# Performance work log

Measured on AMD Instinct MI355X. Metric: run time of the kernel, lower is better.

The kernel has to match this reference:

```python
import jax, jax.numpy as jnp
import numpy as np

N = 100000      # nodes
E = 1600000     # edges (avg degree 16)
F_IN = 64       # in_channels
H = 64          # hidden_channels
L = 3           # num_layers
FINAL = H * L   # jk='cat'


def setup_inputs() -> dict:
    key = jax.random.key(0)
    ks = jax.random.split(key, 16)

    def w(k, i, o):
        return (jax.random.normal(k, (i, o), jnp.float32) / np.sqrt(i)).astype(jnp.float32)

    x = jax.random.normal(ks[0], (N, F_IN), jnp.float32)
    edge_index = jax.random.randint(ks[1], (2, E), 0, N, dtype=jnp.int32)

    inp = {
        'x': x,
        'edge_index': edge_index,
        # layer 1 (in -> H): lin_l (neighbors, with bias), lin_r (root, no bias)
        'W1l': w(ks[2], F_IN, H), 'b1': jnp.zeros((H,), jnp.float32), 'W1r': w(ks[3], F_IN, H),
        # layer 2 (H -> H)
        'W2l': w(ks[4], H, H), 'b2': jnp.zeros((H,), jnp.float32), 'W2r': w(ks[5], H, H),
        # layer 3 (H -> H)
        'W3l': w(ks[6], H, H), 'b3': jnp.zeros((H,), jnp.float32), 'W3r': w(ks[7], H, H),
        # final linear on JK-concat
        'Wlin': w(ks[8], FINAL, 1), 'blin': jnp.zeros((1,), jnp.float32),
    }
    return inp


def _sage_conv(x, src, dst, inv_deg, Wl, bl, Wr):
    # gather neighbor features along edges, segment-mean by destination node
    msg = x[src]                                             # [E, F]
    agg = jax.ops.segment_sum(msg, dst, num_segments=N)      # [N, F]
    agg = agg * inv_deg[:, None]                             # mean aggregation
    return agg @ Wl + bl + x @ Wr                            # lin_l(agg) + lin_r(x)


def reference(x, edge_index, W1l, b1, W1r, W2l, b2, W2r, W3l, b3, W3r, Wlin, blin):
    src, dst = edge_index[0], edge_index[1]
    deg = jax.ops.segment_sum(jnp.ones((E,), jnp.float32), dst, num_segments=N)
    inv_deg = 1.0 / jnp.maximum(deg, 1.0)

    xs = []
    h = x
    for (Wl, bl, Wr) in ((W1l, b1, W1r), (W2l, b2, W2r), (W3l, b3, W3r)):
        h = jax.nn.relu(_sage_conv(h, src, dst, inv_deg, Wl, bl, Wr))
        # dropout is identity in eval mode
        xs.append(h)

    hcat = jnp.concatenate(xs, axis=-1)   # JK 'cat' -> [N, H*L]
    out = hcat @ Wlin + blin              # [N, 1]
    return jax.nn.sigmoid(out).reshape(-1)
```

## Files before the change

### kernel.cpp

```cpp
#include <hip/hip_runtime.h>
#include <math.h>

#define N_NODES 100000
#define N_EDGES 1600000
#define HD 64
#define TILE 128
#define NBUCK 128
#define BNODES 1024
#define EPB 4096

typedef unsigned short ushort_t;
typedef __attribute__((ext_vector_type(8))) unsigned short ushort8_t;
typedef __attribute__((ext_vector_type(8))) short short8_t;
typedef __attribute__((ext_vector_type(4))) float float4_t;

__device__ __forceinline__ float bf2f(ushort_t h){
  union{unsigned u; float f;} v; v.u = ((unsigned)h)<<16; return v.f;
}
__device__ __forceinline__ ushort_t f2bf(float f){
  union{float f; unsigned u;} v; v.f=f;
  unsigned b = v.u + 0x7FFF + ((v.u>>16)&1);
  return (ushort_t)(b>>16);
}

__global__ void k_f32_to_bf16(const float* __restrict__ in, ushort_t* __restrict__ out, int n){
  int i = blockIdx.x*blockDim.x + threadIdx.x;
  int idx = i*4;
  if(idx+3<n){
    float4 v = *(const float4*)&in[idx];
    ushort2 a; a.x=f2bf(v.x); a.y=f2bf(v.y);
    ushort2 b; b.x=f2bf(v.z); b.y=f2bf(v.w);
    *(ushort2*)&out[idx] = a;
    *(ushort2*)&out[idx+2] = b;
  } else {
    for(int k=idx;k<n;k++) out[k]=f2bf(in[k]);
  }
}


__global__ __launch_bounds__(512) void k_hist(const int* __restrict__ dst, int* __restrict__ bcnt, int n){
  __shared__ int lh[NBUCK];
  int t=threadIdx.x;
  if(t<NBUCK) lh[t]=0;
  __syncthreads();
  int base = blockIdx.x*EPB;
  #pragma unroll
  for(int j=0;j<8;j++){
    int e = base + t + j*512;
    if(e<n) atomicAdd(&lh[dst[e]>>10], 1);
  }
  __syncthreads();
  if(t<NBUCK && lh[t]) atomicAdd(&bcnt[t], lh[t]);
}

__global__ void k_scan128(const int* __restrict__ bcnt, int* __restrict__ gcur, int* __restrict__ gbase){
  __shared__ int s[NBUCK];
  int t=threadIdx.x;
  int v=bcnt[t]; s[t]=v;
  __syncthreads();
  for(int off=1; off<NBUCK; off<<=1){
    int a=(t>=off)? s[t-off]:0;
    __syncthreads();
    s[t]+=a;
    __syncthreads();
  }
  int excl = s[t]-v;
  gcur[t]=excl;
  gbase[t]=excl;
  if(t==NBUCK-1) gbase[NBUCK]=s[t];
}

__global__ __launch_bounds__(512) void k_reorder(
    const int* __restrict__ src, const int* __restrict__ dst,
    int* __restrict__ gcur, int2* __restrict__ pairs, int n){
  __shared__ int lh[NBUCK];
  __shared__ int lbase[NBUCK];
  int t=threadIdx.x;
  if(t<NBUCK) lh[t]=0;
  __syncthreads();
  int base = blockIdx.x*EPB;
  int bb[8], rr[8], sv[8], dv[8];
  #pragma unroll
  for(int j=0;j<8;j++){
    int e = base + t + j*512;
    if(e<n){
      int d=dst[e];
      int b=d>>10;
      rr[j]=atomicAdd(&lh[b],1);
      bb[j]=b; sv[j]=src[e]; dv[j]=d;
    } else bb[j]=-1;
  }
  __syncthreads();
  if(t<NBUCK && lh[t]) lbase[t]=atomicAdd(&gcur[t], lh[t]);
  __syncthreads();
  #pragma unroll
  for(int j=0;j<8;j++){
    if(bb[j]>=0){
      int pos = lbase[bb[j]] + rr[j];
      pairs[pos] = make_int2(sv[j], dv[j]);
    }
  }
}

__global__ __launch_bounds__(512) void k_bucket_csr(
    const int2* __restrict__ pairs, const int* __restrict__ gbase,
    int* __restrict__ rowptr, float* __restrict__ invdeg,
    int* __restrict__ csr, int nnodes, int nedges){
  __shared__ int cnt[BNODES];
  __shared__ int part[512];
  int t=threadIdx.x, b=blockIdx.x;
  int nb0 = b*BNODES;
  int e0 = gbase[b], e1 = gbase[b+1];
  cnt[t]=0; cnt[t+512]=0;
  __syncthreads();
  for(int e=e0+t; e<e1; e+=512) atomicAdd(&cnt[pairs[e].y - nb0], 1);
  __syncthreads();
  int c0 = cnt[2*t], c1 = cnt[2*t+1];
  part[t] = c0+c1;
  __syncthreads();
  for(int off=1; off<512; off<<=1){
    int a=(t>=off)? part[t-off]:0;
    __syncthreads();
    part[t]+=a;
    __syncthreads();
  }
  int base = part[t]-(c0+c1);
  int ex0 = base, ex1 = base+c0;
  int n_0 = nb0+2*t, n_1 = nb0+2*t+1;
  if(n_0<nnodes){ rowptr[n_0]=e0+ex0; invdeg[n_0]=1.0f/fmaxf((float)c0,1.0f); }
  if(n_1<nnodes){ rowptr[n_1]=e0+ex1; invdeg[n_1]=1.0f/fmaxf((float)c1,1.0f); }
  if(b==0 && t==0) rowptr[nnodes]=nedges;
  cnt[2*t]=ex0; cnt[2*t+1]=ex1;
  __syncthreads();
  for(int e=e0+t; e<e1; e+=512){
    int2 p = pairs[e];
    int pos = atomicAdd(&cnt[p.y - nb0], 1);
    csr[e0+pos] = p.x;
  }
}

__global__ __launch_bounds__(512) void k_gather(
    const ushort_t* __restrict__ hin, ushort_t* __restrict__ agg,
    const int* __restrict__ rowptr, const int* __restrict__ csr,
    const float* __restrict__ invdeg, int nnodes)
{
  int t=threadIdx.x;
  int lane=t&63, wid=t>>6;
  int node=blockIdx.x*8+wid;
  if(node>=nnodes) return;
  int start=rowptr[node], end=rowptr[node+1];
  int slot = lane>>3;
  int c    = lane&7;
  float idg = invdeg[node];
  float acc[8]={0,0,0,0,0,0,0,0};
  for(int e=start; e<end; e+=16){
    int i1 = e + slot, i2 = e + 8 + slot;
    int c1 = i1<end ? i1 : end-1;
    int c2 = i2<end ? i2 : end-1;
    int s1 = csr[c1], s2 = csr[c2];
    ushort8_t v1 = *(const ushort8_t*)&hin[(size_t)s1*HD + c*8];
    ushort8_t v2 = *(const ushort8_t*)&hin[(size_t)s2*HD + c*8];
    float m1 = i1<end ? 1.f : 0.f;
    float m2 = i2<end ? 1.f : 0.f;
    #pragma unroll
    for(int j=0;j<8;j++){
      acc[j] = fmaf(m1, bf2f(v1[j]), acc[j]);
      acc[j] = fmaf(m2, bf2f(v2[j]), acc[j]);
    }
  }
  #pragma unroll
  for(int off=8; off<64; off<<=1){
    #pragma unroll
    for(int j=0;j<8;j++) acc[j] += __shfl_xor(acc[j], off, 64);
  }
  if(slot==0){
    ushort8_t o;
    #pragma unroll
    for(int j=0;j<8;j++) o[j] = f2bf(acc[j]*idg);
    *(ushort8_t*)&agg[(size_t)node*HD + c*8] = o;
  }
}

__global__ __launch_bounds__(256) void k_dense(
    const ushort_t* __restrict__ hin, const ushort_t* __restrict__ agg,
    ushort_t* __restrict__ hout,
    const float* __restrict__ Wl, const float* __restrict__ bvec, const float* __restrict__ Wr,
    const float* __restrict__ wseg, const float* __restrict__ blin,
    float* __restrict__ partial, float* __restrict__ finout,
    int first, int nnodes)
{
  __shared__ ushort_t sWt[64][136];
  __shared__ ushort_t sOut[TILE][72];
  __shared__ float sB[64], sS[64];
  int t = threadIdx.x;
  int n0 = blockIdx.x*TILE;

  {
    int col = t & 63;
    int k0  = (t >> 6) * 32;
    #pragma unroll
    for (int j = 0; j < 32; ++j) {
      int k = k0 + j;
      float wv = (k < 64) ? Wl[k*64 + col] : Wr[(k-64)*64 + col];
      sWt[col][k] = f2bf(wv);
    }
  }
  if(t<64){ sB[t]=bvec[t]; sS[t]=wseg[t]; }
  __syncthreads();

  int lane = t & 63, wv_ = t >> 6;
  int r16 = lane & 15, g4 = lane >> 4;
  int nbase = n0 + wv_*32;

  float4_t acc[2][4];
  #pragma unroll
  for(int mt=0;mt<2;mt++)
    #pragma unroll
    for(int ct=0;ct<4;ct++)
      #pragma unroll
      for(int r=0;r<4;r++) acc[mt][ct][r]=0.f;

  #pragma unroll
  for (int ks = 0; ks < 4; ++ks) {
    const ushort_t* abuf = (ks < 2) ? agg : hin;
    int koff = (ks & 1)*32 + g4*8;
    short8_t aF[2];
    #pragma unroll
    for (int mt = 0; mt < 2; ++mt) {
      int node = nbase + mt*16 + r16;
      if (node >= nnodes) node = nnodes-1;
      aF[mt] = *(const short8_t*)&abuf[(size_t)node*HD + koff];
    }
    #pragma unroll
    for (int ct = 0; ct < 4; ++ct) {
      short8_t bF = *(const short8_t*)&sWt[ct*16 + r16][ks*32 + g4*8];
      acc[0][ct] = __builtin_amdgcn_mfma_f32_16x16x32_bf16(aF[0], bF, acc[0][ct], 0,0,0);
      acc[1][ct] = __builtin_amdgcn_mfma_f32_16x16x32_bf16(aF[1], bF, acc[1][ct], 0,0,0);
    }
  }

  #pragma unroll
  for (int mt = 0; mt < 2; ++mt)
    #pragma unroll
    for (int ct = 0; ct < 4; ++ct) {
      int col = ct*16 + r16;
      #pragma unroll
      for (int r = 0; r < 4; ++r) {
        int row = g4*4 + r;
        float v = fmaxf(acc[mt][ct][r] + sB[col], 0.f);
        sOut[wv_*32 + mt*16 + row][col] = f2bf(v);
      }
    }
  __syncthreads();

  {
    int nl = t >> 1, half = t & 1;
    int node = n0 + nl;
    float p = 0.f;
    #pragma unroll
    for (int i = 0; i < 4; ++i) {
      int c0 = half*32 + i*8;
      ushort8_t v = *(const ushort8_t*)&sOut[nl][c0];
      if (!finout && node < nnodes)
        *(ushort8_t*)&hout[(size_t)node*HD + c0] = v;
      #pragma unroll
      for (int j = 0; j < 8; ++j) p = fmaf(bf2f(v[j]), sS[c0+j], p);
    }
    p += __shfl_xor(p, 1, 64);
    if (half == 0 && node < nnodes) {
      float q = first ? (blin[0] + p) : (partial[node] + p);
      if (finout) finout[node] = 1.0f/(1.0f+expf(-q));
      else partial[node] = q;
    }
  }
}

extern "C" void kernel_launch(void* const* d_in, const int* in_sizes, int n_in,
                              void* d_out, int out_size, void* d_ws, size_t ws_size,
                              hipStream_t stream){
  const float* x    =(const float*)d_in[0];
  const int*   ei   =(const int*)  d_in[1];
  const float* W1l  =(const float*)d_in[2];
  const float* b1   =(const float*)d_in[3];
  const float* W1r  =(const float*)d_in[4];
  const float* W2l  =(const float*)d_in[5];
  const float* b2   =(const float*)d_in[6];
  const float* W2r  =(const float*)d_in[7];
  const float* W3l  =(const float*)d_in[8];
  const float* b3   =(const float*)d_in[9];
  const float* W3r  =(const float*)d_in[10];
  const float* Wlin =(const float*)d_in[11];
  const float* blin =(const float*)d_in[12];
  float* out=(float*)d_out;

  const int N=N_NODES, E=N_EDGES;
  char* ws=(char*)d_ws;
  size_t off=0;
  auto take=[&](size_t bytes)->char*{ char* p=ws+off; off=(off+bytes+255)&~(size_t)255; return p; };
  int*      bcnt     =(int*)     take((size_t)NBUCK*4);
  int*      gcur     =(int*)     take((size_t)NBUCK*4);
  int*      gbase    =(int*)     take((size_t)(NBUCK+1)*4);
  int*      rowptr   =(int*)     take((size_t)(N+1)*4);
  int*      csr      =(int*)     take((size_t)E*4);
  int2*     pairs    =(int2*)    take((size_t)E*8);
  float*    invdeg   =(float*)   take((size_t)N*4);
  ushort_t* xbf      =(ushort_t*)take((size_t)N*HD*2);
  ushort_t* hbfA     =(ushort_t*)take((size_t)N*HD*2);
  ushort_t* hbfB     =(ushort_t*)take((size_t)N*HD*2);
  ushort_t* aggbf    =(ushort_t*)take((size_t)N*HD*2);
  float*    pacc     =(float*)   take((size_t)N*4);

  const int RB=(E+EPB-1)/EPB;
  const int CB=(N*HD/4+255)/256;
  const int BB=(N+BNODES-1)/BNODES;

  hipMemsetAsync(bcnt, 0, (size_t)NBUCK*4, stream);
  k_f32_to_bf16<<<CB, 256, 0, stream>>>(x, xbf, N*HD);
  k_hist       <<<RB, 512, 0, stream>>>(ei+E, bcnt, E);
  k_scan128    <<<1, NBUCK, 0, stream>>>(bcnt, gcur, gbase);
  k_reorder    <<<RB, 512, 0, stream>>>(ei, ei+E, gcur, pairs, E);
  k_bucket_csr <<<BB, 512, 0, stream>>>(pairs, gbase, rowptr, invdeg, csr, N, E);

  dim3 gg((N+7)/8);
  dim3 gd((N+TILE-1)/TILE);

  k_gather<<<gg, 512, 0, stream>>>(xbf, aggbf, rowptr, csr, invdeg, N);
  k_dense <<<gd, 256, 0, stream>>>(xbf, aggbf, hbfA, W1l,b1,W1r, Wlin+0,  blin, pacc, (float*)nullptr, 1, N);
  k_gather<<<gg, 512, 0, stream>>>(hbfA, aggbf, rowptr, csr, invdeg, N);
  k_dense <<<gd, 256, 0, stream>>>(hbfA, aggbf, hbfB, W2l,b2,W2r, Wlin+64, blin, pacc, (float*)nullptr, 0, N);
  k_gather<<<gg, 512, 0, stream>>>(hbfB, aggbf, rowptr, csr, invdeg, N);
  k_dense <<<gd, 256, 0, stream>>>(hbfB, aggbf, hbfA, W3l,b3,W3r, Wlin+128, blin, pacc, out, 0, N);
}
```

Baseline: 220.3 us.

## Gather neighbor features from FP8 copies and pack edge pairs into one int

The edge gather in each layer now reads an FP8 (e4m3) copy of the node features instead of bf16, which halves the bytes fetched per neighbor. The x-conversion kernel and the dense kernel write that FP8 copy next to the bf16 copy. Separately, the bucket-sort pairs are packed into a single 32-bit int (src in the low 17 bits, local dst offset in the high bits), which halves that intermediate traffic. The cost is extra FP8 writes in the dense kernels and a loss of precision in neighbor aggregation, which could affect tolerance.

Result: no change. 217.8 us (-1.1%).

```diff
diff --git a/kernel.cpp b/kernel.cpp
--- a/kernel.cpp
+++ b/kernel.cpp
@@ -10,9 +10,11 @@
 #define EPB 4096
 
 typedef unsigned short ushort_t;
+typedef unsigned char uchar_t;
 typedef __attribute__((ext_vector_type(8))) unsigned short ushort8_t;
 typedef __attribute__((ext_vector_type(8))) short short8_t;
 typedef __attribute__((ext_vector_type(4))) float float4_t;
+typedef __attribute__((ext_vector_type(2))) float float2_t;
 
 __device__ __forceinline__ float bf2f(ushort_t h){
   union{unsigned u; float f;} v; v.u = ((unsigned)h)<<16; return v.f;
@@ -23,17 +25,25 @@
   return (ushort_t)(b>>16);
 }
 
-__global__ void k_f32_to_bf16(const float* __restrict__ in, ushort_t* __restrict__ out, int n){
+__global__ void k_convert_x(const float* __restrict__ in, ushort_t* __restrict__ obf,
+                            uchar_t* __restrict__ o8, int n){
   int i = blockIdx.x*blockDim.x + threadIdx.x;
   int idx = i*4;
   if(idx+3<n){
     float4 v = *(const float4*)&in[idx];
     ushort2 a; a.x=f2bf(v.x); a.y=f2bf(v.y);
     ushort2 b; b.x=f2bf(v.z); b.y=f2bf(v.w);
-    *(ushort2*)&out[idx] = a;
-    *(ushort2*)&out[idx+2] = b;
+    *(ushort2*)&obf[idx] = a;
+    *(ushort2*)&obf[idx+2] = b;
+    int p = __builtin_amdgcn_cvt_pk_fp8_f32(v.x, v.y, 0, false);
+    p     = __builtin_amdgcn_cvt_pk_fp8_f32(v.z, v.w, p, true);
+    *(unsigned int*)&o8[idx] = (unsigned int)p;
   } else {
-    for(int k=idx;k<n;k++) out[k]=f2bf(in[k]);
+    for(int k=idx;k<n;k++){
+      obf[k]=f2bf(in[k]);
+      int p = __builtin_amdgcn_cvt_pk_fp8_f32(in[k], 0.f, 0, false);
+      o8[k] = (uchar_t)(p & 0xFF);
+    }
   }
 }
 
@@ -72,14 +82,14 @@
 
 __global__ __launch_bounds__(512) void k_reorder(
     const int* __restrict__ src, const int* __restrict__ dst,
-    int* __restrict__ gcur, int2* __restrict__ pairs, int n){
+    int* __restrict__ gcur, int* __restrict__ pairs, int n){
   __shared__ int lh[NBUCK];
   __shared__ int lbase[NBUCK];
   int t=threadIdx.x;
   if(t<NBUCK) lh[t]=0;
   __syncthreads();
   int base = blockIdx.x*EPB;
-  int bb[8], rr[8], sv[8], dv[8];
+  int bb[8], rr[8], pv[8];
   #pragma unroll
   for(int j=0;j<8;j++){
     int e = base + t + j*512;
@@ -87,7 +97,8 @@
       int d=dst[e];
       int b=d>>10;
       rr[j]=atomicAdd(&lh[b],1);
-      bb[j]=b; sv[j]=src[e]; dv[j]=d;
+      bb[j]=b;
+      pv[j]=src[e] | ((d & 1023)<<17);
     } else bb[j]=-1;
   }
   __syncthreads();
@@ -97,13 +108,13 @@
   for(int j=0;j<8;j++){
     if(bb[j]>=0){
       int pos = lbase[bb[j]] + rr[j];
-      pairs[pos] = make_int2(sv[j], dv[j]);
+      pairs[pos] = pv[j];
     }
   }
 }
 
 __global__ __launch_bounds__(512) void k_bucket_csr(
-    const int2* __restrict__ pairs, const int* __restrict__ gbase,
+    const int* __restrict__ pairs, const int* __restrict__ gbase,
     int* __restrict__ rowptr, float* __restrict__ invdeg,
     int* __restrict__ csr, int nnodes, int nedges){
   __shared__ int cnt[BNODES];
@@ -113,7 +124,7 @@
   int e0 = gbase[b], e1 = gbase[b+1];
   cnt[t]=0; cnt[t+512]=0;
   __syncthreads();
-  for(int e=e0+t; e<e1; e+=512) atomicAdd(&cnt[pairs[e].y - nb0], 1);
+  for(int e=e0+t; e<e1; e+=512) atomicAdd(&cnt[pairs[e]>>17], 1);
   __syncthreads();
   int c0 = cnt[2*t], c1 = cnt[2*t+1];
   part[t] = c0+c1;
@@ -133,14 +144,14 @@
   cnt[2*t]=ex0; cnt[2*t+1]=ex1;
   __syncthreads();
   for(int e=e0+t; e<e1; e+=512){
-    int2 p = pairs[e];
-    int pos = atomicAdd(&cnt[p.y - nb0], 1);
-    csr[e0+pos] = p.x;
+    int p = pairs[e];
+    int pos = atomicAdd(&cnt[p>>17], 1);
+    csr[e0+pos] = p & 0x1FFFF;
   }
 }
 
 __global__ __launch_bounds__(512) void k_gather(
-    const ushort_t* __restrict__ hin, ushort_t* __restrict__ agg,
+    const uchar_t* __restrict__ hin8, ushort_t* __restrict__ agg,
     const int* __restrict__ rowptr, const int* __restrict__ csr,
     const float* __restrict__ invdeg, int nnodes)
 {
@@ -158,15 +169,19 @@
     int c1 = i1<end ? i1 : end-1;
     int c2 = i2<end ? i2 : end-1;
     int s1 = csr[c1], s2 = csr[c2];
-    ushort8_t v1 = *(const ushort8_t*)&hin[(size_t)s1*HD + c*8];
-    ushort8_t v2 = *(const ushort8_t*)&hin[(size_t)s2*HD + c*8];
+    uint2 u1 = *(const uint2*)&hin8[(size_t)s1*HD + c*8];
+    uint2 u2 = *(const uint2*)&hin8[(size_t)s2*HD + c*8];
     float m1 = i1<end ? 1.f : 0.f;
     float m2 = i2<end ? 1.f : 0.f;
-    #pragma unroll
-    for(int j=0;j<8;j++){
-      acc[j] = fmaf(m1, bf2f(v1[j]), acc[j]);
-      acc[j] = fmaf(m2, bf2f(v2[j]), acc[j]);
-    }
+    float2_t f;
+    f = __builtin_amdgcn_cvt_pk_f32_fp8((int)u1.x, false); acc[0]=fmaf(m1,f.x,acc[0]); acc[1]=fmaf(m1,f.y,acc[1]);
+    f = __builtin_amdgcn_cvt_pk_f32_fp8((int)u1.x, true ); acc[2]=fmaf(m1,f.x,acc[2]); acc[3]=fmaf(m1,f.y,acc[3]);
+    f = __builtin_amdgcn_cvt_pk_f32_fp8((int)u1.y, false); acc[4]=fmaf(m1,f.x,acc[4]); acc[5]=fmaf(m1,f.y,acc[5]);
+    f = __builtin_amdgcn_cvt_pk_f32_fp8((int)u1.y, true ); acc[6]=fmaf(m1,f.x,acc[6]); acc[7]=fmaf(m1,f.y,acc[7]);
+    f = __builtin_amdgcn_cvt_pk_f32_fp8((int)u2.x, false); acc[0]=fmaf(m2,f.x,acc[0]); acc[1]=fmaf(m2,f.y,acc[1]);
+    f = __builtin_amdgcn_cvt_pk_f32_fp8((int)u2.x, true ); acc[2]=fmaf(m2,f.x,acc[2]); acc[3]=fmaf(m2,f.y,acc[3]);
+    f = __builtin_amdgcn_cvt_pk_f32_fp8((int)u2.y, false); acc[4]=fmaf(m2,f.x,acc[4]); acc[5]=fmaf(m2,f.y,acc[5]);
+    f = __builtin_amdgcn_cvt_pk_f32_fp8((int)u2.y, true ); acc[6]=fmaf(m2,f.x,acc[6]); acc[7]=fmaf(m2,f.y,acc[7]);
   }
   #pragma unroll
   for(int off=8; off<64; off<<=1){
@@ -183,7 +198,7 @@
 
 __global__ __launch_bounds__(256) void k_dense(
     const ushort_t* __restrict__ hin, const ushort_t* __restrict__ agg,
-    ushort_t* __restrict__ hout,
+    ushort_t* __restrict__ hout, uchar_t* __restrict__ h8out,
     const float* __restrict__ Wl, const float* __restrict__ bvec, const float* __restrict__ Wr,
     const float* __restrict__ wseg, const float* __restrict__ blin,
     float* __restrict__ partial, float* __restrict__ finout,
@@ -261,10 +276,18 @@
     for (int i = 0; i < 4; ++i) {
       int c0 = half*32 + i*8;
       ushort8_t v = *(const ushort8_t*)&sOut[nl][c0];
-      if (!finout && node < nnodes)
+      float fv[8];
+      #pragma unroll
+      for (int j = 0; j < 8; ++j){ fv[j]=bf2f(v[j]); p = fmaf(fv[j], sS[c0+j], p); }
+      if (!finout && node < nnodes){
         *(ushort8_t*)&hout[(size_t)node*HD + c0] = v;
-      #pragma unroll
-      for (int j = 0; j < 8; ++j) p = fmaf(bf2f(v[j]), sS[c0+j], p);
+        int q0 = __builtin_amdgcn_cvt_pk_fp8_f32(fv[0], fv[1], 0, false);
+        q0     = __builtin_amdgcn_cvt_pk_fp8_f32(fv[2], fv[3], q0, true);
+        int q1 = __builtin_amdgcn_cvt_pk_fp8_f32(fv[4], fv[5], 0, false);
+        q1     = __builtin_amdgcn_cvt_pk_fp8_f32(fv[6], fv[7], q1, true);
+        uint2 st; st.x=(unsigned)q0; st.y=(unsigned)q1;
+        *(uint2*)&h8out[(size_t)node*HD + c0] = st;
+      }
     }
     p += __shfl_xor(p, 1, 64);
     if (half == 0 && node < nnodes) {
@@ -302,12 +325,15 @@
   int*      gbase    =(int*)     take((size_t)(NBUCK+1)*4);
   int*      rowptr   =(int*)     take((size_t)(N+1)*4);
   int*      csr      =(int*)     take((size_t)E*4);
-  int2*     pairs    =(int2*)    take((size_t)E*8);
+  int*      pairs    =(int*)     take((size_t)E*4);
   float*    invdeg   =(float*)   take((size_t)N*4);
   ushort_t* xbf      =(ushort_t*)take((size_t)N*HD*2);
   ushort_t* hbfA     =(ushort_t*)take((size_t)N*HD*2);
   ushort_t* hbfB     =(ushort_t*)take((size_t)N*HD*2);
   ushort_t* aggbf    =(ushort_t*)take((size_t)N*HD*2);
+  uchar_t*  x8       =(uchar_t*) take((size_t)N*HD);
+  uchar_t*  h8A      =(uchar_t*) take((size_t)N*HD);
+  uchar_t*  h8B      =(uchar_t*) take((size_t)N*HD);
   float*    pacc     =(float*)   take((size_t)N*4);
 
   const int RB=(E+EPB-1)/EPB;
@@ -315,7 +341,7 @@
   const int BB=(N+BNODES-1)/BNODES;
 
   hipMemsetAsync(bcnt, 0, (size_t)NBUCK*4, stream);
-  k_f32_to_bf16<<<CB, 256, 0, stream>>>(x, xbf, N*HD);
+  k_convert_x  <<<CB, 256, 0, stream>>>(x, xbf, x8, N*HD);
   k_hist       <<<RB, 512, 0, stream>>>(ei+E, bcnt, E);
   k_scan128    <<<1, NBUCK, 0, stream>>>(bcnt, gcur, gbase);
   k_reorder    <<<RB, 512, 0, stream>>>(ei, ei+E, gcur, pairs, E);
@@ -324,10 +350,10 @@
   dim3 gg((N+7)/8);
   dim3 gd((N+TILE-1)/TILE);
 
-  k_gather<<<gg, 512, 0, stream>>>(xbf, aggbf, rowptr, csr, invdeg, N);
-  k_dense <<<gd, 256, 0, stream>>>(xbf, aggbf, hbfA, W1l,b1,W1r, Wlin+0,  blin, pacc, (float*)nullptr, 1, N);
-  k_gather<<<gg, 512, 0, stream>>>(hbfA, aggbf, rowptr, csr, invdeg, N);
-  k_dense <<<gd, 256, 0, stream>>>(hbfA, aggbf, hbfB, W2l,b2,W2r, Wlin+64, blin, pacc, (float*)nullptr, 0, N);
-  k_gather<<<gg, 512, 0, stream>>>(hbfB, aggbf, rowptr, csr, invdeg, N);
-  k_dense <<<gd, 256, 0, stream>>>(hbfB, aggbf, hbfA, W3l,b3,W3r, Wlin+128, blin, pacc, out, 0, N);
-}
+  k_gather<<<gg, 512, 0, stream>>>(x8,  aggbf, rowptr, csr, invdeg, N);
+  k_dense <<<gd, 256, 0, stream>>>(xbf,  aggbf, hbfA, h8A, W1l,b1,W1r, Wlin+0,   blin, pacc, (float*)nullptr, 1, N);
+  k_gather<<<gg, 512, 0, stream>>>(h8A, aggbf, rowptr, csr, invdeg, N);
+  k_dense <<<gd, 256, 0, stream>>>(hbfA, aggbf, hbfB, h8B, W2l,b2,W2r, Wlin+64,  blin, pacc, (float*)nullptr, 0, N);
+  k_gather<<<gg, 512, 0, stream>>>(h8B, aggbf, rowptr, csr, invdeg, N);
+  k_dense <<<gd, 256, 0, stream>>>(hbfB, aggbf, hbfA, h8A, W3l,b3,W3r, Wlin+128, blin, pacc, out, 0, N);
+}
```
